# Kernel tuning notes

Hardware: AMD Instinct MI355X
Metric: run time of the kernel (lower is better)

The kernel has to match this reference:

```python
import jax, jax.numpy as jnp
import numpy as np

# problem constants (from config / init_kwargs)
OBJ = 1024        # object_size
D = 256           # diffraction_size == probe_size (pad = 0)
P = 256           # probe_size
S = 8             # num_slices
B = 256           # batch of scan indices
NSCAN = 4096      # number of scan positions
PX = 0.1          # pixel_size (Angstrom)
LAM = 0.0197      # wavelength (Angstrom, ~300 kV)
CONV = 0.025      # convergence angle (rad)
DZ = 2.0          # slice thickness (Angstrom)


def _freq_grids():
    f = jnp.fft.fftfreq(D, d=PX).astype(jnp.float32)
    kx, ky = jnp.meshgrid(f, f, indexing='ij')
    return kx, ky


def _probe(defocus, Cs, astig_mag, astig_angle, aperture_smooth):
    kx, ky = _freq_grids()
    k = jnp.sqrt(kx ** 2 + ky ** 2)
    k_angle = jnp.arctan2(ky, kx)
    chi = (np.pi * LAM * defocus * k ** 2
           + 0.5 * np.pi * LAM ** 3 * (Cs * 1e6) * k ** 4
           + np.pi * LAM * astig_mag * k ** 2 * jnp.cos(2.0 * (k_angle - astig_angle)))
    k_max = CONV / LAM
    smooth = jnp.abs(aperture_smooth) + 0.01
    aperture = jax.nn.sigmoid((k_max - k) / (k_max * smooth))
    probe_k = aperture.astype(jnp.complex64) * jnp.exp(1j * chi.astype(jnp.complex64))
    probe_real = jnp.fft.ifftshift(jnp.fft.ifft2(probe_k))
    probe_real = probe_real / jnp.sqrt(jnp.sum(jnp.abs(probe_real) ** 2))
    # crop(P) with P == D and c == h is the identity slice [0:D, 0:D]
    return probe_real


def _propagator():
    kx, ky = _freq_grids()
    k2 = kx ** 2 + ky ** 2
    return jnp.exp(1j * (np.pi * LAM * DZ * k2).astype(jnp.complex64))


def setup_inputs() -> dict:
    key = jax.random.key(0)
    k1, k2, k3, k4 = jax.random.split(key, 4)
    slice_amp = jnp.ones((S, OBJ, OBJ), dtype=jnp.float32) \
        + 0.05 * jax.random.normal(k1, (S, OBJ, OBJ), dtype=jnp.float32)
    slice_phase = 0.1 * jax.random.normal(k2, (S, OBJ, OBJ), dtype=jnp.float32)
    scan_positions = jax.random.randint(k3, (NSCAN, 2), 0, OBJ - P, dtype=jnp.int32)
    indices = jax.random.randint(k4, (B,), 0, NSCAN, dtype=jnp.int32)
    return {
        'slice_amp': slice_amp,
        'slice_phase': slice_phase,
        'defocus': jnp.float32(50.0),
        'Cs': jnp.float32(0.5),
        'astig_mag': jnp.float32(10.0),
        'astig_angle': jnp.float32(0.0),
        'aperture_smooth': jnp.float32(0.1),
        'scan_positions': scan_positions,
        'indices': indices,
    }


def reference(slice_amp, slice_phase, defocus, Cs, astig_mag, astig_angle,
              aperture_smooth, scan_positions, indices):
    probe = _probe(defocus, Cs, astig_mag, astig_angle, aperture_smooth)  # [D,D] c64
    H = _propagator()                                                      # [D,D] c64
    pos = scan_positions[indices]                                          # [B,2] (y,x)

    def gather_patch(t, yx):
        return jax.lax.dynamic_slice(t, (yx[0], yx[1]), (P, P))

    wave = jnp.broadcast_to(probe[None, :, :], (B, P, P))  # [B,P,P] c64
    for s in range(S):  # small fixed slice recurrence
        t = slice_amp[s].astype(jnp.complex64) * jnp.exp(1j * slice_phase[s].astype(jnp.complex64))
        patches = jax.vmap(gather_patch, in_axes=(None, 0))(t, pos)  # [B,P,P]
        exit_wave = wave * patches                      # pad = 0 since P == D
        wave = jnp.fft.ifft2(jnp.fft.fft2(exit_wave) * H)
    psi = jnp.fft.fft2(wave)                            # [B,D,D] complex64
    return psi
```

## Files before the change

kernel.cpp:

```cpp
#include <hip/hip_runtime.h>
#include <hip/hip_fp16.h>
#include <math.h>

typedef unsigned short u16;
typedef unsigned int   u32;

__device__ __forceinline__ bool is_f64(const void* amp){
  u32 u = ((const u32*)amp)[1];
  return ((u >> 20) & 0xFFF) >= 0x3FB;
}
__device__ __forceinline__ bool is_i64(const void* spos){
  const u32* p = (const u32*)spos;
  return (p[1] | p[3] | p[5]) == 0;
}
__device__ __forceinline__ float ldf(const void* p, size_t i, bool f64){
  return f64 ? (float)((const double*)p)[i] : ((const float*)p)[i];
}
__device__ __forceinline__ double lds_scalar(const void* p, bool f64){
  return f64 ? ((const double*)p)[0] : (double)((const float*)p)[0];
}
__device__ __forceinline__ int ldi(const void* p, size_t i, bool i64){
  return i64 ? (int)((const long long*)p)[i] : ((const int*)p)[i];
}

__device__ __forceinline__ u16 f2bf(float f){
  u32 u = __float_as_uint(f);
  u32 r = 0x7fffu + ((u >> 16) & 1u);
  return (u16)((u + r) >> 16);
}
__device__ __forceinline__ void stout(void* p, size_t i, float2 v){
  ((u32*)p)[i] = (u32)f2bf(v.y) | ((u32)f2bf(v.x) << 16);
}

template<int H>
__device__ __forceinline__ float2 ld_state(const void* p, size_t i){
  if (H){
    __half2 h = ((const __half2*)p)[i];
    return __half22float2(h);
  }
  return ((const float2*)p)[i];
}
template<int H>
__device__ __forceinline__ void st_state(void* p, size_t i, float2 v){
  if (H) ((__half2*)p)[i] = __floats2half2_rn(v.x, v.y);
  else   ((float2*)p)[i] = v;
}

__device__ __forceinline__ float2 cadd(float2 a, float2 b){ return make_float2(a.x+b.x, a.y+b.y); }
__device__ __forceinline__ float2 csub(float2 a, float2 b){ return make_float2(a.x-b.x, a.y-b.y); }
__device__ __forceinline__ float2 cmul(float2 a, float2 b){ return make_float2(a.x*b.x - a.y*b.y, a.x*b.y + a.y*b.x); }
__device__ __forceinline__ float2 cmulc(float2 a, float2 b){ return make_float2(a.x*b.x + a.y*b.y, a.y*b.x - a.x*b.y); }
__device__ __forceinline__ float2 cscale(float2 a, float s){ return make_float2(a.x*s, a.y*s); }

template<int SGN>
__device__ __forceinline__ void fft4(float2& a, float2& b, float2& c, float2& d){
  float2 apc = cadd(a,c), amc = csub(a,c);
  float2 bpd = cadd(b,d), bmd = csub(b,d);
  float2 jb = (SGN < 0) ? make_float2(bmd.y, -bmd.x) : make_float2(-bmd.y, bmd.x);
  a = cadd(apc, bpd);
  b = cadd(amc, jb);
  c = csub(apc, bpd);
  d = csub(amc, jb);
}
template<int SGN>
__device__ __forceinline__ float2 twc(float2 z, float re, float im){
  float i2 = (SGN < 0) ? im : -im;
  return make_float2(z.x*re - z.y*i2, z.x*i2 + z.y*re);
}
template<int SGN>
__device__ __forceinline__ void fft16(float2 v[16]){
  float2 h[16];
#pragma unroll
  for (int n1=0;n1<4;n1++){
    float2 a=v[n1], b=v[n1+4], c=v[n1+8], d=v[n1+12];
    fft4<SGN>(a,b,c,d);
    h[n1*4+0]=a; h[n1*4+1]=b; h[n1*4+2]=c; h[n1*4+3]=d;
  }
  const float C1=0.92387953251f, S1=0.38268343236f, C2=0.70710678119f;
  h[5]  = twc<SGN>(h[5],  C1,-S1);
  h[6]  = twc<SGN>(h[6],  C2,-C2);
  h[7]  = twc<SGN>(h[7],  S1,-C1);
  h[9]  = twc<SGN>(h[9],  C2,-C2);
  h[10] = twc<SGN>(h[10], 0.f,-1.f);
  h[11] = twc<SGN>(h[11],-C2,-C2);
  h[13] = twc<SGN>(h[13], S1,-C1);
  h[14] = twc<SGN>(h[14],-C2,-C2);
  h[15] = twc<SGN>(h[15],-C1, S1);
#pragma unroll
  for (int q=0;q<4;q++){
    float2 a=h[q], b=h[4+q], c=h[8+q], d=h[12+q];
    fft4<SGN>(a,b,c,d);
    v[q]=a; v[q+4]=b; v[q+8]=c; v[q+12]=d;
  }
}

__device__ __forceinline__ void make_tw(float2 tw[15], int t){
  float s0, c0;
  sincosf(0.0245436926f * (float)t, &s0, &c0);
  float2 w1 = make_float2(c0, -s0);
  tw[0] = w1;
#pragma unroll
  for (int q=1;q<15;q++) tw[q] = cmul(tw[q-1], w1);
}

template<int SGN, int BARRIER>
__device__ __forceinline__ void fft256(float2 v[16], float* Tr, float* Ti, int g, int t,
                                       const float2 tw[15]){
  fft16<SGN>(v);
#pragma unroll
  for (int q=1;q<16;q++){
    v[q] = (SGN < 0) ? cmul(v[q], tw[q-1]) : cmulc(v[q], tw[q-1]);
  }
  int base = g*257;
  if (BARRIER) __syncthreads();
#pragma unroll
  for (int k1=0;k1<16;k1++){
    int o = base + t*16 + (k1^t);
    Tr[o] = v[k1].x; Ti[o] = v[k1].y;
  }
  if (BARRIER) __syncthreads();
#pragma unroll
  for (int n1=0;n1<16;n1++){
    int o = base + n1*16 + (t^n1);
    v[n1] = make_float2(Tr[o], Ti[o]);
  }
  fft16<SGN>(v);
  if (SGN > 0){
#pragma unroll
    for (int q=0;q<16;q++) v[q] = cscale(v[q], 1.f/256.f);
  }
}

__device__ __forceinline__ float ffreq(int i){ return (float)(i < 128 ? i : i - 256) * 0.0390625f; }

#define LDS_F 4112
#define KMAX  1.26903553299f
#define PHCONST 0.123778191f


__global__ void __launch_bounds__(256) probe_rowsF(const void* defocus, const void* Cs,
                                                   const void* astig_mag, const void* astig_angle,
                                                   const void* ap_smooth, const void* ampflag,
                                                   float2* tmp){
  __shared__ float Tr[LDS_F], Ti[LDS_F];
  bool f64 = is_f64(ampflag);
  int tid = threadIdx.x, g = tid>>4, t = tid&15;
  int r = blockIdx.x*16 + g;
  double df = lds_scalar(defocus, f64), cs = lds_scalar(Cs, f64);
  double am = lds_scalar(astig_mag, f64), aa = lds_scalar(astig_angle, f64);
  float sm = fabsf((float)lds_scalar(ap_smooth, f64)) + 0.01f;
  const double LAMd = 0.0197;
  float kxv = ffreq(r);
  float2 v[16];
#pragma unroll
  for (int j=0;j<16;j++){
    int c = t + 16*j;
    float kyv = ffreq(c);
    double k2 = (double)kxv*kxv + (double)kyv*kyv;
    float k  = sqrtf((float)k2);
    double ang = atan2((double)kyv, (double)kxv);
    double chi = M_PI*LAMd*df*k2
               + 0.5*M_PI*LAMd*LAMd*LAMd*(cs*1e6)*k2*k2
               + M_PI*LAMd*am*k2*cos(2.0*(ang - aa));
    float ap = 1.f/(1.f + expf(-(KMAX - k)/(KMAX*sm)));
    double sc = sin(chi), cc = cos(chi);
    v[j] = make_float2(ap*(float)cc, ap*(float)sc);
  }
  float2 tw[15]; make_tw(tw, t);
  fft256<1,0>(v, Tr, Ti, g, t, tw);
#pragma unroll
  for (int j=0;j<16;j++) tmp[(r<<8) + t + 16*j] = v[j];
}

__global__ void __launch_bounds__(256) probe_colsF(const float2* tmp, float2* probe_out,
                                                   const void* ap_smooth, const void* ampflag){
  __shared__ float Tr[LDS_F], Ti[LDS_F];
  bool f64 = is_f64(ampflag);
  int tid = threadIdx.x, xl = tid&15, t = tid>>4;
  int cx = blockIdx.x*16 + xl;
  float sm = fabsf((float)lds_scalar(ap_smooth, f64)) + 0.01f;
  float S = 0.f;
  for (int i = tid; i < 65536; i += 256){
    float kx = ffreq(i>>8), ky = ffreq(i&255);
    float k = sqrtf(kx*kx + ky*ky);
    float ap = 1.f/(1.f + expf(-(KMAX - k)/(KMAX*sm)));
    S += ap*ap;
  }
#pragma unroll
  for (int off=32; off>0; off>>=1) S += __shfl_down(S, off);
  if ((tid&63)==0) Tr[tid>>6] = S;
  __syncthreads();
  float scale = 256.f * rsqrtf(Tr[0]+Tr[1]+Tr[2]+Tr[3]);
  float2 v[16];
#pragma unroll
  for (int j=0;j<16;j++) v[j] = tmp[((t+16*j)<<8) + cx];
  float2 tw[15]; make_tw(tw, t);
  fft256<1,1>(v, Tr, Ti, xl, t, tw);
  int csh = (cx + 128) & 255;
#pragma unroll
  for (int j=0;j<16;j++){
    int y = t + 16*j;
    probe_out[(((y+128)&255)<<8) + csh] = cscale(v[j], scale);
  }
}

__global__ void __launch_bounds__(256) build_ttabF(const void* amp, const void* phase,
                                                   float2* ttab){
  bool f64 = is_f64(amp);
  int tid = threadIdx.x;
#pragma unroll
  for (int k=0;k<4;k++){
    size_t i = (size_t)blockIdx.x*1024 + tid + 256*k;
    float A = ldf(amp, i, f64);
    float P = ldf(phase, i, f64);
    float sp, cp; sincosf(P, &sp, &cp);
    ttab[i] = make_float2(A*cp, A*sp);
  }
}

template<int H>
__global__ void __launch_bounds__(256) row_passT(const void* amp, const void* phase,
                                                 const void* spos, const void* sidx,
                                                 void* state, const float2* probe,
                                                 const float2* ttab, int s, int first,
                                                 int use_tt){
  __shared__ float Tr[LDS_F], Ti[LDS_F];
  bool f64 = is_f64(amp);
  bool i64 = is_i64(spos);
  int tid = threadIdx.x, g = tid>>4, t = tid&15;
  int b = blockIdx.y;
  int y = blockIdx.x*16 + g;
  int n = ldi(sidx, b, i64);
  int py = ldi(spos, 2*(size_t)n, i64), px = ldi(spos, 2*(size_t)n+1, i64);
  size_t rowbase = ((size_t)s<<20) + (size_t)(py+y)*1024 + px;
  float2 tv[16];
  if (use_tt){
#pragma unroll
    for (int j=0;j<16;j++) tv[j] = ttab[rowbase + t + 16*j];
  } else {
#pragma unroll
    for (int j=0;j<16;j++){
      int x = t + 16*j;
      float A = ldf(amp,   rowbase + x, f64);
      float P = ldf(phase, rowbase + x, f64);
      float sp, cp; sincosf(P, &sp, &cp);
      tv[j] = make_float2(A*cp, A*sp);
    }
  }
  size_t ib = (size_t)b << 16;
  float2 tw[15]; make_tw(tw, t);
  float2 v[16];
  if (first){
#pragma unroll
    for (int j=0;j<16;j++) v[j] = probe[(y<<8) + t + 16*j];
  } else {
#pragma unroll
    for (int j=0;j<16;j++) v[j] = ld_state<H>(state, ib + (y<<8) + t + 16*j);
    fft256<1,0>(v, Tr, Ti, g, t, tw);
  }
#pragma unroll
  for (int j=0;j<16;j++) v[j] = cmul(v[j], tv[j]);
  fft256<-1,0>(v, Tr, Ti, g, t, tw);
#pragma unroll
  for (int j=0;j<16;j++) st_state<H>(state, ib + (y<<8) + t + 16*j, v[j]);
}

template<int H>
__global__ void __launch_bounds__(256) col_passT(void* state){
  __shared__ float Tr[LDS_F], Ti[LDS_F];
  __shared__ float2 h1[256];
  int tid = threadIdx.x, xl = tid&15, t = tid>>4;
  int b = blockIdx.y;
  int cx = blockIdx.x*16 + xl;
  size_t ib = (size_t)b << 16;
  {
    float kk = ffreq(tid);
    float a = PHCONST * kk * kk;
    float sa, ca; sincosf(a, &sa, &ca);
    h1[tid] = make_float2(ca, sa);
  }
  float2 tw[15]; make_tw(tw, t);
  float2 v[16];
#pragma unroll
  for (int j=0;j<16;j++) v[j] = ld_state<H>(state, ib + ((t+16*j)<<8) + cx);
  fft256<-1,1>(v, Tr, Ti, xl, t, tw);
  float2 hx = h1[cx & 255];
#pragma unroll
  for (int j=0;j<16;j++) v[j] = cmul(v[j], cmul(h1[t + 16*j], hx));
  fft256<1,1>(v, Tr, Ti, xl, t, tw);
#pragma unroll
  for (int j=0;j<16;j++) st_state<H>(state, ib + ((t+16*j)<<8) + cx, v[j]);
}

template<int H>
__global__ void __launch_bounds__(256) col_finT(void* state, void* outp){
  __shared__ float Tr[LDS_F], Ti[LDS_F];
  __shared__ float2 h1[256];
  int tid = threadIdx.x, xl = tid&15, t = tid>>4;
  int b = blockIdx.y;
  int cx = blockIdx.x*16 + xl;
  size_t ib = (size_t)b << 16;
  {
    float kk = ffreq(tid);
    float a = PHCONST * kk * kk;
    float sa, ca; sincosf(a, &sa, &ca);
    h1[tid] = make_float2(ca, sa);
  }
  float2 tw[15]; make_tw(tw, t);
  float2 v[16];
#pragma unroll
  for (int j=0;j<16;j++) v[j] = ld_state<H>(state, ib + ((t+16*j)<<8) + cx);
  fft256<-1,1>(v, Tr, Ti, xl, t, tw);
  float2 hx = h1[cx & 255];
#pragma unroll
  for (int j=0;j<16;j++){
    float2 r = cmul(v[j], cmul(h1[t + 16*j], hx));
    stout(outp, ib + ((t+16*j)<<8) + cx, r);
  }
}

template<int H>
static void run_new(const void* amp, const void* phase,
                    const void* df, const void* cs, const void* am, const void* aa,
                    const void* sm, const void* spos, const void* sidx, int B,
                    void* state, float2* ttab, int use_tt,
                    void* dout, hipStream_t stream){
  char* dob = (char*)dout;
  float2* probe = (float2*)dob;
  float2* ptmp  = (float2*)(dob + 524288);
  probe_rowsF<<<16, 256, 0, stream>>>(df, cs, am, aa, sm, amp, ptmp);
  probe_colsF<<<16, 256, 0, stream>>>(ptmp, probe, sm, amp);
  if (use_tt) build_ttabF<<<8192, 256, 0, stream>>>(amp, phase, ttab);
  dim3 grid(16, B);
  row_passT<H><<<grid, 256, 0, stream>>>(amp, phase, spos, sidx, state, probe, ttab, 0, 1, use_tt);
  col_passT<H><<<grid, 256, 0, stream>>>(state);
  for (int s = 1; s < 7; s++){
    row_passT<H><<<grid, 256, 0, stream>>>(amp, phase, spos, sidx, state, probe, ttab, s, 0, use_tt);
    col_passT<H><<<grid, 256, 0, stream>>>(state);
  }
  row_passT<H><<<grid, 256, 0, stream>>>(amp, phase, spos, sidx, state, probe, ttab, 7, 0, use_tt);
  col_finT<H><<<grid, 256, 0, stream>>>(state, dout);
}

extern "C" void kernel_launch(void* const* d_in, const int* in_sizes, int n_in,
                              void* d_out, int out_size, void* d_ws, size_t ws_size,
                              hipStream_t stream) {
  const void* amp   = d_in[0];
  const void* phase = d_in[1];
  const void* df    = d_in[2];
  const void* cs    = d_in[3];
  const void* am    = d_in[4];
  const void* aa    = d_in[5];
  const void* sm    = d_in[6];
  const void* spos  = d_in[7];
  const void* sidx  = d_in[8];
  int B = in_sizes[8];
  (void)out_size; (void)n_in;

  size_t stateH = (size_t)B * 65536 * 4;
  const size_t ttabB = (size_t)8 * 1024 * 1024 * 8;
  if (ws_size >= stateH + ttabB){
    void*   state = d_ws;
    float2* ttab  = (float2*)((char*)d_ws + stateH);
    run_new<1>(amp, phase, df, cs, am, aa, sm, spos, sidx, B,
               state, ttab, 1, d_out, stream);
  } else if (ws_size >= stateH){
    run_new<1>(amp, phase, df, cs, am, aa, sm, spos, sidx, B,
               d_ws, (float2*)d_ws, 0, d_out, stream);
  } else {
    run_new<1>(amp, phase, df, cs, am, aa, sm, spos, sidx, B,
               d_out, (float2*)d_out, 0, d_out, stream);
  }
}
```

Measured before the change: 838.9 us.

## Use half-precision LDS transposes, shared twiddle tables, and folded FFT scaling

The FFT transpose buffer moves from two fp32 shared arrays to one __half2 array, halving LDS footprint and traffic, which may raise occupancy. Per-thread twiddle generation by recursive multiplication is replaced with a 240-entry shared table built with sincosf. The 1/256 inverse-FFT normalisation is dropped from the inner FFTs and folded into the transmission table, the propagator and the probe scale. The main risks are lost accuracy from fp16 intermediates and overflow or underflow from the changed scaling.

```diff
diff --git a/kernel.cpp b/kernel.cpp
--- a/kernel.cpp
+++ b/kernel.cpp
@@ -94,46 +94,48 @@
   }
 }
 
-__device__ __forceinline__ void make_tw(float2 tw[15], int t){
-  float s0, c0;
-  sincosf(0.0245436926f * (float)t, &s0, &c0);
-  float2 w1 = make_float2(c0, -s0);
-  tw[0] = w1;
-#pragma unroll
-  for (int q=1;q<15;q++) tw[q] = cmul(tw[q-1], w1);
-}
-
-template<int SGN, int BARRIER>
-__device__ __forceinline__ void fft256(float2 v[16], float* Tr, float* Ti, int g, int t,
-                                       const float2 tw[15]){
+#define LDS_T 4112
+#define ISC   (1.f/256.f)
+
+__device__ __forceinline__ void fill_tw(float2* twl, int tid){
+  if (tid < 240){
+    int tt = tid / 15, q = tid - tt*15 + 1;
+    float s, c; sincosf(0.0245436926f * (float)(tt*q), &s, &c);
+    twl[tid] = make_float2(c, -s);
+  }
+}
+
+template<int SGN, int BARRIER, int SCALE>
+__device__ __forceinline__ void fft256p(float2 v[16], __half2* T, const float2* twt,
+                                        int g, int t){
   fft16<SGN>(v);
 #pragma unroll
   for (int q=1;q<16;q++){
-    v[q] = (SGN < 0) ? cmul(v[q], tw[q-1]) : cmulc(v[q], tw[q-1]);
+    float2 w = twt[q-1];
+    v[q] = (SGN < 0) ? cmul(v[q], w) : cmulc(v[q], w);
   }
   int base = g*257;
   if (BARRIER) __syncthreads();
 #pragma unroll
   for (int k1=0;k1<16;k1++){
     int o = base + t*16 + (k1^t);
-    Tr[o] = v[k1].x; Ti[o] = v[k1].y;
+    T[o] = __floats2half2_rn(v[k1].x, v[k1].y);
   }
   if (BARRIER) __syncthreads();
 #pragma unroll
   for (int n1=0;n1<16;n1++){
     int o = base + n1*16 + (t^n1);
-    v[n1] = make_float2(Tr[o], Ti[o]);
+    v[n1] = __half22float2(T[o]);
   }
   fft16<SGN>(v);
-  if (SGN > 0){
-#pragma unroll
-    for (int q=0;q<16;q++) v[q] = cscale(v[q], 1.f/256.f);
+  if (SGN > 0 && SCALE){
+#pragma unroll
+    for (int q=0;q<16;q++) v[q] = cscale(v[q], ISC);
   }
 }
 
 __device__ __forceinline__ float ffreq(int i){ return (float)(i < 128 ? i : i - 256) * 0.0390625f; }
 
-#define LDS_F 4112
 #define KMAX  1.26903553299f
 #define PHCONST 0.123778191f
 
@@ -142,9 +144,11 @@
                                                    const void* astig_mag, const void* astig_angle,
                                                    const void* ap_smooth, const void* ampflag,
                                                    float2* tmp){
-  __shared__ float Tr[LDS_F], Ti[LDS_F];
+  __shared__ __half2 T[LDS_T];
+  __shared__ float2 twl[240];
   bool f64 = is_f64(ampflag);
   int tid = threadIdx.x, g = tid>>4, t = tid&15;
+  fill_tw(twl, tid);
   int r = blockIdx.x*16 + g;
   double df = lds_scalar(defocus, f64), cs = lds_scalar(Cs, f64);
   double am = lds_scalar(astig_mag, f64), aa = lds_scalar(astig_angle, f64);
@@ -166,17 +170,20 @@
     double sc = sin(chi), cc = cos(chi);
     v[j] = make_float2(ap*(float)cc, ap*(float)sc);
   }
-  float2 tw[15]; make_tw(tw, t);
-  fft256<1,0>(v, Tr, Ti, g, t, tw);
+  __syncthreads();
+  fft256p<1,0,1>(v, T, twl + t*15, g, t);
 #pragma unroll
   for (int j=0;j<16;j++) tmp[(r<<8) + t + 16*j] = v[j];
 }
 
 __global__ void __launch_bounds__(256) probe_colsF(const float2* tmp, float2* probe_out,
                                                    const void* ap_smooth, const void* ampflag){
-  __shared__ float Tr[LDS_F], Ti[LDS_F];
+  __shared__ __half2 T[LDS_T];
+  __shared__ float2 twl[240];
+  __shared__ float Ssum[4];
   bool f64 = is_f64(ampflag);
   int tid = threadIdx.x, xl = tid&15, t = tid>>4;
+  fill_tw(twl, tid);
   int cx = blockIdx.x*16 + xl;
   float sm = fabsf((float)lds_scalar(ap_smooth, f64)) + 0.01f;
   float S = 0.f;
@@ -188,14 +195,13 @@
   }
 #pragma unroll
   for (int off=32; off>0; off>>=1) S += __shfl_down(S, off);
-  if ((tid&63)==0) Tr[tid>>6] = S;
-  __syncthreads();
-  float scale = 256.f * rsqrtf(Tr[0]+Tr[1]+Tr[2]+Tr[3]);
+  if ((tid&63)==0) Ssum[tid>>6] = S;
+  __syncthreads();
+  float scale = 65536.f * rsqrtf(Ssum[0]+Ssum[1]+Ssum[2]+Ssum[3]);
   float2 v[16];
 #pragma unroll
   for (int j=0;j<16;j++) v[j] = tmp[((t+16*j)<<8) + cx];
-  float2 tw[15]; make_tw(tw, t);
-  fft256<1,1>(v, Tr, Ti, xl, t, tw);
+  fft256p<1,1,1>(v, T, twl + t*15, xl, t);
   int csh = (cx + 128) & 255;
 #pragma unroll
   for (int j=0;j<16;j++){
@@ -214,7 +220,7 @@
     float A = ldf(amp, i, f64);
     float P = ldf(phase, i, f64);
     float sp, cp; sincosf(P, &sp, &cp);
-    ttab[i] = make_float2(A*cp, A*sp);
+    ttab[i] = make_float2(A*cp*ISC, A*sp*ISC);
   }
 }
 
@@ -224,10 +230,12 @@
                                                  void* state, const float2* probe,
                                                  const float2* ttab, int s, int first,
                                                  int use_tt){
-  __shared__ float Tr[LDS_F], Ti[LDS_F];
+  __shared__ __half2 T[LDS_T];
+  __shared__ float2 twl[240];
   bool f64 = is_f64(amp);
   bool i64 = is_i64(spos);
   int tid = threadIdx.x, g = tid>>4, t = tid&15;
+  fill_tw(twl, tid);
   int b = blockIdx.y;
   int y = blockIdx.x*16 + g;
   int n = ldi(sidx, b, i64);
@@ -244,11 +252,10 @@
       float A = ldf(amp,   rowbase + x, f64);
       float P = ldf(phase, rowbase + x, f64);
       float sp, cp; sincosf(P, &sp, &cp);
-      tv[j] = make_float2(A*cp, A*sp);
+      tv[j] = make_float2(A*cp*ISC, A*sp*ISC);
     }
   }
   size_t ib = (size_t)b << 16;
-  float2 tw[15]; make_tw(tw, t);
   float2 v[16];
   if (first){
 #pragma unroll
@@ -256,61 +263,66 @@
   } else {
 #pragma unroll
     for (int j=0;j<16;j++) v[j] = ld_state<H>(state, ib + (y<<8) + t + 16*j);
-    fft256<1,0>(v, Tr, Ti, g, t, tw);
-  }
+  }
+  __syncthreads();
+  if (!first) fft256p<1,0,0>(v, T, twl + t*15, g, t);
 #pragma unroll
   for (int j=0;j<16;j++) v[j] = cmul(v[j], tv[j]);
-  fft256<-1,0>(v, Tr, Ti, g, t, tw);
+  fft256p<-1,0,0>(v, T, twl + t*15, g, t);
 #pragma unroll
   for (int j=0;j<16;j++) st_state<H>(state, ib + (y<<8) + t + 16*j, v[j]);
 }
 
 template<int H>
 __global__ void __launch_bounds__(256) col_passT(void* state){
-  __shared__ float Tr[LDS_F], Ti[LDS_F];
+  __shared__ __half2 T[LDS_T];
+  __shared__ float2 twl[240];
   __shared__ float2 h1[256];
   int tid = threadIdx.x, xl = tid&15, t = tid>>4;
+  fill_tw(twl, tid);
+  {
+    float kk = ffreq(tid);
+    float a = PHCONST * kk * kk;
+    float sa, ca; sincosf(a, &sa, &ca);
+    h1[tid] = make_float2(ca*0.0625f, sa*0.0625f);
+  }
   int b = blockIdx.y;
   int cx = blockIdx.x*16 + xl;
   size_t ib = (size_t)b << 16;
+  float2 v[16];
+#pragma unroll
+  for (int j=0;j<16;j++) v[j] = ld_state<H>(state, ib + ((t+16*j)<<8) + cx);
+  __syncthreads();
+  fft256p<-1,1,0>(v, T, twl + t*15, xl, t);
+  float2 hx = h1[cx & 255];
+#pragma unroll
+  for (int j=0;j<16;j++) v[j] = cmul(v[j], cmul(h1[t + 16*j], hx));
+  fft256p<1,1,0>(v, T, twl + t*15, xl, t);
+#pragma unroll
+  for (int j=0;j<16;j++) st_state<H>(state, ib + ((t+16*j)<<8) + cx, v[j]);
+}
+
+template<int H>
+__global__ void __launch_bounds__(256) col_finT(void* state, void* outp){
+  __shared__ __half2 T[LDS_T];
+  __shared__ float2 twl[240];
+  __shared__ float2 h1[256];
+  int tid = threadIdx.x, xl = tid&15, t = tid>>4;
+  fill_tw(twl, tid);
   {
     float kk = ffreq(tid);
     float a = PHCONST * kk * kk;
     float sa, ca; sincosf(a, &sa, &ca);
     h1[tid] = make_float2(ca, sa);
   }
-  float2 tw[15]; make_tw(tw, t);
-  float2 v[16];
-#pragma unroll
-  for (int j=0;j<16;j++) v[j] = ld_state<H>(state, ib + ((t+16*j)<<8) + cx);
-  fft256<-1,1>(v, Tr, Ti, xl, t, tw);
-  float2 hx = h1[cx & 255];
-#pragma unroll
-  for (int j=0;j<16;j++) v[j] = cmul(v[j], cmul(h1[t + 16*j], hx));
-  fft256<1,1>(v, Tr, Ti, xl, t, tw);
-#pragma unroll
-  for (int j=0;j<16;j++) st_state<H>(state, ib + ((t+16*j)<<8) + cx, v[j]);
-}
-
-template<int H>
-__global__ void __launch_bounds__(256) col_finT(void* state, void* outp){
-  __shared__ float Tr[LDS_F], Ti[LDS_F];
-  __shared__ float2 h1[256];
-  int tid = threadIdx.x, xl = tid&15, t = tid>>4;
   int b = blockIdx.y;
   int cx = blockIdx.x*16 + xl;
   size_t ib = (size_t)b << 16;
-  {
-    float kk = ffreq(tid);
-    float a = PHCONST * kk * kk;
-    float sa, ca; sincosf(a, &sa, &ca);
-    h1[tid] = make_float2(ca, sa);
-  }
-  float2 tw[15]; make_tw(tw, t);
   float2 v[16];
 #pragma unroll
   for (int j=0;j<16;j++) v[j] = ld_state<H>(state, ib + ((t+16*j)<<8) + cx);
-  fft256<-1,1>(v, Tr, Ti, xl, t, tw);
+  __syncthreads();
+  fft256p<-1,1,0>(v, T, twl + t*15, xl, t);
   float2 hx = h1[cx & 255];
 #pragma unroll
   for (int j=0;j<16;j++){
```

New measurement: 887.3 us. 5.8% more time.
